# Performance work log

Hardware: AMD Instinct MI355X
Metric: run time of the kernel (lower is better)

Reference implementation:

```python
import jax, jax.numpy as jnp
import numpy as np

K = 3          # kernel_size
STRIDE = 1
ITERS = 3      # num_iterations


def squash(t, axis=-1):
    sn = jnp.sum(t * t, axis=axis, keepdims=True)
    return (sn / (1.0 + sn)) * t / jnp.sqrt(sn)


def setup_inputs() -> dict:
    key = jax.random.key(0)
    k1, k2 = jax.random.split(key)
    B, Nin, H, Cin = 8, 32, 14, 8
    C, Cout = 32, 16
    R = Nin * K * K  # 288 route nodes
    x = jax.random.normal(k1, (B, Nin, H, H, Cin), dtype=jnp.float32)
    route_weights = jax.random.normal(k2, (C, R, Cin, Cout), dtype=jnp.float32)
    return {"x": x, "route_weights": route_weights}


def reference(x, route_weights):
    B, Nin, H, _, Cin = x.shape
    C, R, _, Cout = route_weights.shape
    w = (H - K) // STRIDE + 1

    # Extract all w*w spatial windows at once (instead of the python loop).
    rows = STRIDE * jnp.arange(w)[:, None] + jnp.arange(K)  # [w, K]
    win = x[:, :, rows]            # [B, Nin, w, K, W, Cin]
    win = win[:, :, :, :, rows]    # [B, Nin, w, K, w, K, Cin]
    # route-node order matches .view: (Nin, k, k) flattened
    win = win.transpose(0, 2, 4, 1, 3, 5, 6).reshape(B, w, w, R, Cin)

    priors = jnp.einsum('bpqri,crio->cbpqro', win, route_weights)

    # Dynamic routing (fixed small iteration count -> python loop is fine).
    logits = jnp.zeros_like(priors)
    out = None
    for i in range(ITERS):
        probs = jax.nn.softmax(logits, axis=4)  # softmax over route nodes (dim=2 in torch 5D layout)
        out = squash(jnp.sum(probs * priors, axis=4, keepdims=True))  # [C,B,w,w,1,Cout]
        if i != ITERS - 1:
            logits = logits + jnp.sum(priors * out, axis=-1, keepdims=True)

    out = out[:, :, :, :, 0, :]          # [C, B, w, w, Cout]
    return out.transpose(1, 0, 2, 3, 4)  # [B, C, w, w, Cout]
```

## Files before the change

kernel.cpp:

```cpp
#include <hip/hip_runtime.h>
#include <math.h>

namespace {
constexpr int NIN   = 32;
constexpr int H_    = 14;
constexpr int CIN   = 8;
constexpr int C_    = 32;
constexpr int COUT  = 16;
constexpr int R_    = 288;
constexpr int W_    = 12;
constexpr int NITER = 3;
constexpr int CH    = 32;
constexpr int NCH   = 9;
constexpr size_t XSUB = (size_t)NIN * H_ * H_ * CIN;
}

typedef unsigned int u32;
typedef const __attribute__((address_space(1))) u32* as1_u32p;
typedef __attribute__((address_space(3))) u32* as3_u32p;

__device__ __forceinline__ void async_copy16(const void* g, void* l) {
    __builtin_amdgcn_global_load_lds((as1_u32p)g, (as3_u32p)l, 16, 0, 0);
}
__device__ __forceinline__ float dot4(const float4 a, const float4 b) {
    return fmaf(a.x, b.x, fmaf(a.y, b.y, fmaf(a.z, b.z, a.w * b.w)));
}
__device__ __forceinline__ float dpp_add_xor1(float v) {
    int t = __builtin_amdgcn_update_dpp(0, __float_as_int(v), 0xB1, 0xF, 0xF, true);
    return v + __int_as_float(t);
}
__device__ __forceinline__ float dpp_add_xor2(float v) {
    int t = __builtin_amdgcn_update_dpp(0, __float_as_int(v), 0x4E, 0xF, 0xF, true);
    return v + __int_as_float(t);
}
__device__ __forceinline__ float dpp_add_shr4(float v) {
    int t = __builtin_amdgcn_update_dpp(0, __float_as_int(v), 0x114, 0xF, 0xF, true);
    return v + __int_as_float(t);
}
__device__ __forceinline__ float dpp_add_shr8(float v) {
    int t = __builtin_amdgcn_update_dpp(0, __float_as_int(v), 0x118, 0xF, 0xF, true);
    return v + __int_as_float(t);
}
template <int CTRL>
__device__ __forceinline__ float dpp_bc(float v) {
    return __int_as_float(
        __builtin_amdgcn_update_dpp(0, __float_as_int(v), CTRL, 0xF, 0xF, true));
}

__global__ __launch_bounds__(256)
void caps_routeC(const float* __restrict__ x,
                 const float* __restrict__ rw,
                 float* __restrict__ out)
{
    const int tid = threadIdx.x;
    const int p  = blockIdx.x / W_;
    const int q  = blockIdx.x % W_;
    const int b0 = blockIdx.y * 4;
    const int c  = blockIdx.z;

    __shared__ float4 wbuf[2][1024];
    __shared__ float  sRed[2][4][2][16];
    __shared__ float  redE[2][4][2];

    const int og   = tid & 3;
    const int rl   = tid >> 2;
    const int cr   = rl & 31;
    const int sh   = rl >> 5;
    const int lane = tid & 63;
    const int wv   = tid >> 6;
    const int sA   = sh * 2;

    const float* xq = x + (size_t)(b0 + sA + (og >> 1)) * XSUB + (og & 1) * 4;
    const float4* rwcF4 = (const float4*)(rw + (size_t)c * R_ * CIN * COUT);

    float4 xvb[2];
    auto xld = [&](int k, int slot) {
        const int r  = k * CH + cr;
        const int n  = r / 9, rem = r - n * 9;
        const int kh = rem / 3, kw = rem - kh * 3;
        xvb[slot] = *(const float4*)(xq + ((n * H_ + (p + kh)) * H_ + (q + kw)) * CIN);
    };

    auto stage = [&](int k, int buf) {
        const float4* gchunk = rwcF4 + (size_t)k * (CH * 32);
        #pragma unroll
        for (int t = 0; t < 4; ++t) {
            const int s   = t * 256 + tid;
            const int ii  = s >> 7;
            const int wcr = (s >> 2) & 31;
            async_copy16(gchunk + (wcr * 32 + ii * 4 + (s & 3)),
                         (char*)&wbuf[buf][0] + (t * 256 + (tid & 192)) * 16);
        }
    };

    float4 acc[NCH][2];

    xld(0, 0);
    xld(1, 1);
    stage(0, 0);
    #pragma unroll
    for (int k = 0; k < NCH; ++k) {
        __syncthreads();
        if (k + 1 < NCH) stage(k + 1, (k + 1) & 1);
        const float4 cur = xvb[k & 1];
        float fA[8], fB[8];
        fA[0] = dpp_bc<0x00>(cur.x); fA[1] = dpp_bc<0x00>(cur.y);
        fA[2] = dpp_bc<0x00>(cur.z); fA[3] = dpp_bc<0x00>(cur.w);
        fA[4] = dpp_bc<0x55>(cur.x); fA[5] = dpp_bc<0x55>(cur.y);
        fA[6] = dpp_bc<0x55>(cur.z); fA[7] = dpp_bc<0x55>(cur.w);
        fB[0] = dpp_bc<0xAA>(cur.x); fB[1] = dpp_bc<0xAA>(cur.y);
        fB[2] = dpp_bc<0xAA>(cur.z); fB[3] = dpp_bc<0xAA>(cur.w);
        fB[4] = dpp_bc<0xFF>(cur.x); fB[5] = dpp_bc<0xFF>(cur.y);
        fB[6] = dpp_bc<0xFF>(cur.z); fB[7] = dpp_bc<0xFF>(cur.w);
        if (k + 2 < NCH) xld(k + 2, k & 1);
        const float4* wb = &wbuf[k & 1][0];
        float4 a0 = make_float4(0.f, 0.f, 0.f, 0.f);
        float4 a1 = make_float4(0.f, 0.f, 0.f, 0.f);
        #pragma unroll
        for (int i = 0; i < 8; ++i) {
            const float4 wv4 = wb[i * 128 + cr * 4 + og];
            a0.x = fmaf(fA[i], wv4.x, a0.x);  a1.x = fmaf(fB[i], wv4.x, a1.x);
            a0.y = fmaf(fA[i], wv4.y, a0.y);  a1.y = fmaf(fB[i], wv4.y, a1.y);
            a0.z = fmaf(fA[i], wv4.z, a0.z);  a1.z = fmaf(fB[i], wv4.z, a1.z);
            a0.w = fmaf(fA[i], wv4.w, a0.w);  a1.w = fmaf(fB[i], wv4.w, a1.w);
        }
        acc[k][0] = a0;  acc[k][1] = a1;
    }

    float lgA[NCH], lgB[NCH];
    #pragma unroll
    for (int j = 0; j < NCH; ++j) { lgA[j] = 0.f; lgB[j] = 0.f; }

    float4 v0, v1;

    for (int it = 0; it < NITER; ++it) {
        const int par = it & 1;
        float4 s0 = make_float4(0.f, 0.f, 0.f, 0.f);
        float4 s1 = make_float4(0.f, 0.f, 0.f, 0.f);
        float se0 = 0.f, se1 = 0.f;

        if (it == 0) {
            #pragma unroll
            for (int j = 0; j < NCH; ++j) {
                s0.x += acc[j][0].x;  s1.x += acc[j][1].x;
                s0.y += acc[j][0].y;  s1.y += acc[j][1].y;
                s0.z += acc[j][0].z;  s1.z += acc[j][1].z;
                s0.w += acc[j][0].w;  s1.w += acc[j][1].w;
            }
        } else {
            #pragma unroll
            for (int j = 0; j < NCH; ++j) {
                float d0 = dot4(acc[j][0], v0);
                float d1 = dot4(acc[j][1], v1);
                d0 = dpp_add_xor1(d0);  d1 = dpp_add_xor1(d1);
                d0 = dpp_add_xor2(d0);  d1 = dpp_add_xor2(d1);
                lgA[j] += d0;                 lgB[j] += d1;
                const float e0 = __expf(lgA[j]);
                const float e1 = __expf(lgB[j]);
                se0 += e0;                    se1 += e1;
                s0.x = fmaf(e0, acc[j][0].x, s0.x);  s1.x = fmaf(e1, acc[j][1].x, s1.x);
                s0.y = fmaf(e0, acc[j][0].y, s0.y);  s1.y = fmaf(e1, acc[j][1].y, s1.y);
                s0.z = fmaf(e0, acc[j][0].z, s0.z);  s1.z = fmaf(e1, acc[j][1].z, s1.z);
                s0.w = fmaf(e0, acc[j][0].w, s0.w);  s1.w = fmaf(e1, acc[j][1].w, s1.w);
            }
            se0 = dpp_add_shr4(se0);  se1 = dpp_add_shr4(se1);
            se0 = dpp_add_shr8(se0);  se1 = dpp_add_shr8(se1);
            se0 += __shfl_xor(se0, 16, 64);  se1 += __shfl_xor(se1, 16, 64);
            se0 += __shfl_xor(se0, 32, 64);  se1 += __shfl_xor(se1, 32, 64);
            if (lane == 15) { redE[par][wv][0] = se0; redE[par][wv][1] = se1; }
        }

        s0.x = dpp_add_shr4(s0.x);  s1.x = dpp_add_shr4(s1.x);
        s0.y = dpp_add_shr4(s0.y);  s1.y = dpp_add_shr4(s1.y);
        s0.z = dpp_add_shr4(s0.z);  s1.z = dpp_add_shr4(s1.z);
        s0.w = dpp_add_shr4(s0.w);  s1.w = dpp_add_shr4(s1.w);
        s0.x = dpp_add_shr8(s0.x);  s1.x = dpp_add_shr8(s1.x);
        s0.y = dpp_add_shr8(s0.y);  s1.y = dpp_add_shr8(s1.y);
        s0.z = dpp_add_shr8(s0.z);  s1.z = dpp_add_shr8(s1.z);
        s0.w = dpp_add_shr8(s0.w);  s1.w = dpp_add_shr8(s1.w);
        #pragma unroll
        for (int off = 16; off <= 32; off <<= 1) {
            s0.x += __shfl_xor(s0.x, off, 64);  s1.x += __shfl_xor(s1.x, off, 64);
            s0.y += __shfl_xor(s0.y, off, 64);  s1.y += __shfl_xor(s1.y, off, 64);
            s0.z += __shfl_xor(s0.z, off, 64);  s1.z += __shfl_xor(s1.z, off, 64);
            s0.w += __shfl_xor(s0.w, off, 64);  s1.w += __shfl_xor(s1.w, off, 64);
        }
        if (lane >= 12 && lane < 16) {
            *(float4*)&sRed[par][wv][0][(lane & 3) * 4] = s0;
            *(float4*)&sRed[par][wv][1][(lane & 3) * 4] = s1;
        }
        __syncthreads();

        const float4 pa0 = *(const float4*)&sRed[par][sh * 2    ][0][og * 4];
        const float4 pb0 = *(const float4*)&sRed[par][sh * 2 + 1][0][og * 4];
        const float4 pa1 = *(const float4*)&sRed[par][sh * 2    ][1][og * 4];
        const float4 pb1 = *(const float4*)&sRed[par][sh * 2 + 1][1][og * 4];
        float inv0, inv1;
        if (it == 0) {
            inv0 = inv1 = 1.0f / (float)R_;
        } else {
            inv0 = 1.0f / (redE[par][sh * 2][0] + redE[par][sh * 2 + 1][0]);
            inv1 = 1.0f / (redE[par][sh * 2][1] + redE[par][sh * 2 + 1][1]);
        }
        float4 sc0, sc1;
        sc0.x = (pa0.x + pb0.x) * inv0;  sc1.x = (pa1.x + pb1.x) * inv1;
        sc0.y = (pa0.y + pb0.y) * inv0;  sc1.y = (pa1.y + pb1.y) * inv1;
        sc0.z = (pa0.z + pb0.z) * inv0;  sc1.z = (pa1.z + pb1.z) * inv1;
        sc0.w = (pa0.w + pb0.w) * inv0;  sc1.w = (pa1.w + pb1.w) * inv1;
        float sn0 = dot4(sc0, sc0);
        float sn1 = dot4(sc1, sc1);
        sn0 = dpp_add_xor1(sn0);  sn1 = dpp_add_xor1(sn1);
        sn0 = dpp_add_xor2(sn0);  sn1 = dpp_add_xor2(sn1);
        const float f0 = sqrtf(sn0) / (1.0f + sn0);
        const float f1 = sqrtf(sn1) / (1.0f + sn1);
        v0.x = sc0.x * f0;  v1.x = sc1.x * f1;
        v0.y = sc0.y * f0;  v1.y = sc1.y * f1;
        v0.z = sc0.z * f0;  v1.z = sc1.z * f1;
        v0.w = sc0.w * f0;  v1.w = sc1.w * f1;
    }

    if (cr == 0) {
        *(float4*)&out[((((size_t)(b0 + sA)     * C_ + c) * W_ + p) * W_ + q) * COUT + og * 4] = v0;
        *(float4*)&out[((((size_t)(b0 + sA + 1) * C_ + c) * W_ + p) * W_ + q) * COUT + og * 4] = v1;
    }
}

extern "C" void kernel_launch(void* const* d_in, const int* in_sizes, int n_in,
                              void* d_out, int out_size, void* d_ws, size_t ws_size,
                              hipStream_t stream) {
    const float* x  = (const float*)d_in[0];
    const float* rw = (const float*)d_in[1];
    float* out = (float*)d_out;
    dim3 grid(W_ * W_, 2, C_);
    caps_routeC<<<grid, 256, 0, stream>>>(x, rw, out);
}
```

Before: 197.9 us.

## Deepen weight staging to a five-buffer half-chunk pipeline with explicit vmcnt waits

The weight staging loop is split into 18 half-chunks held in a 5-slot shared-memory ring with four stages in flight. Hand-tuned s_waitcnt vmcnt values and raw s_barrier calls replace __syncthreads, and sched_barrier fences pin the instruction order. The aim is to hide global-to-LDS load latency behind the FMA work with less stalling per barrier. The reduction scratch now aliases the ring buffer, and the hard-coded wait counts depend on the exact order the compiler emits memory instructions, so a codegen change could break correctness.

```diff
diff --git a/kernel.cpp b/kernel.cpp
--- a/kernel.cpp
+++ b/kernel.cpp
@@ -12,6 +12,7 @@
 constexpr int NITER = 3;
 constexpr int CH    = 32;
 constexpr int NCH   = 9;
+constexpr int NPH   = 18;
 constexpr size_t XSUB = (size_t)NIN * H_ * H_ * CIN;
 }
 
@@ -58,9 +59,9 @@
     const int b0 = blockIdx.y * 4;
     const int c  = blockIdx.z;
 
-    __shared__ float4 wbuf[2][1024];
-    __shared__ float  sRed[2][4][2][16];
-    __shared__ float  redE[2][4][2];
+    __shared__ __align__(16) char smem[40960];
+    float (*sRedP)[4][2][16] = reinterpret_cast<float (*)[4][2][16]>(smem);
+    float (*redEP)[4][2]     = reinterpret_cast<float (*)[4][2]>(smem + 1024);
 
     const int og   = tid & 3;
     const int rl   = tid >> 2;
@@ -81,50 +82,73 @@
         xvb[slot] = *(const float4*)(xq + ((n * H_ + (p + kh)) * H_ + (q + kw)) * CIN);
     };
 
-    auto stage = [&](int k, int buf) {
+    auto stage = [&](int h) {
+        const int k = h >> 1, half = h & 1, buf = h % 5;
         const float4* gchunk = rwcF4 + (size_t)k * (CH * 32);
         #pragma unroll
-        for (int t = 0; t < 4; ++t) {
+        for (int t = 0; t < 2; ++t) {
             const int s   = t * 256 + tid;
             const int ii  = s >> 7;
             const int wcr = (s >> 2) & 31;
-            async_copy16(gchunk + (wcr * 32 + ii * 4 + (s & 3)),
-                         (char*)&wbuf[buf][0] + (t * 256 + (tid & 192)) * 16);
+            async_copy16(gchunk + (wcr * 32 + (half * 4 + ii) * 4 + (s & 3)),
+                         smem + buf * 8192 + (t * 256 + (tid & 192)) * 16);
         }
     };
 
+    constexpr int NWAIT[NPH] = {6,7,7,8, 7,8,7,8, 7,8,7,8, 7,9,8,6, 2,0};
+    auto vwait = [](int n) {
+        switch (n) {
+          case 2: asm volatile("s_waitcnt vmcnt(2) lgkmcnt(0)" ::: "memory"); break;
+          case 6: asm volatile("s_waitcnt vmcnt(6) lgkmcnt(0)" ::: "memory"); break;
+          case 7: asm volatile("s_waitcnt vmcnt(7) lgkmcnt(0)" ::: "memory"); break;
+          case 8: asm volatile("s_waitcnt vmcnt(8) lgkmcnt(0)" ::: "memory"); break;
+          case 9: asm volatile("s_waitcnt vmcnt(9) lgkmcnt(0)" ::: "memory"); break;
+          default: asm volatile("s_waitcnt vmcnt(0) lgkmcnt(0)" ::: "memory"); break;
+        }
+    };
+
     float4 acc[NCH][2];
+    float  fA[8], fB[8];
+    float4 a0, a1;
 
     xld(0, 0);
-    xld(1, 1);
-    stage(0, 0);
+    stage(0); stage(1); stage(2); stage(3);
     #pragma unroll
-    for (int k = 0; k < NCH; ++k) {
-        __syncthreads();
-        if (k + 1 < NCH) stage(k + 1, (k + 1) & 1);
-        const float4 cur = xvb[k & 1];
-        float fA[8], fB[8];
-        fA[0] = dpp_bc<0x00>(cur.x); fA[1] = dpp_bc<0x00>(cur.y);
-        fA[2] = dpp_bc<0x00>(cur.z); fA[3] = dpp_bc<0x00>(cur.w);
-        fA[4] = dpp_bc<0x55>(cur.x); fA[5] = dpp_bc<0x55>(cur.y);
-        fA[6] = dpp_bc<0x55>(cur.z); fA[7] = dpp_bc<0x55>(cur.w);
-        fB[0] = dpp_bc<0xAA>(cur.x); fB[1] = dpp_bc<0xAA>(cur.y);
-        fB[2] = dpp_bc<0xAA>(cur.z); fB[3] = dpp_bc<0xAA>(cur.w);
-        fB[4] = dpp_bc<0xFF>(cur.x); fB[5] = dpp_bc<0xFF>(cur.y);
-        fB[6] = dpp_bc<0xFF>(cur.z); fB[7] = dpp_bc<0xFF>(cur.w);
-        if (k + 2 < NCH) xld(k + 2, k & 1);
-        const float4* wb = &wbuf[k & 1][0];
-        float4 a0 = make_float4(0.f, 0.f, 0.f, 0.f);
-        float4 a1 = make_float4(0.f, 0.f, 0.f, 0.f);
+    for (int h = 0; h < NPH; ++h) {
+        const int k = h >> 1, half = h & 1;
+        vwait(NWAIT[h]);
+        __builtin_amdgcn_s_barrier();
+        __builtin_amdgcn_sched_barrier(0);
+        if (half == 0) {
+            const float4 cur = xvb[k & 1];
+            fA[0] = dpp_bc<0x00>(cur.x); fA[1] = dpp_bc<0x00>(cur.y);
+            fA[2] = dpp_bc<0x00>(cur.z); fA[3] = dpp_bc<0x00>(cur.w);
+            fA[4] = dpp_bc<0x55>(cur.x); fA[5] = dpp_bc<0x55>(cur.y);
+            fA[6] = dpp_bc<0x55>(cur.z); fA[7] = dpp_bc<0x55>(cur.w);
+            fB[0] = dpp_bc<0xAA>(cur.x); fB[1] = dpp_bc<0xAA>(cur.y);
+            fB[2] = dpp_bc<0xAA>(cur.z); fB[3] = dpp_bc<0xAA>(cur.w);
+            fB[4] = dpp_bc<0xFF>(cur.x); fB[5] = dpp_bc<0xFF>(cur.y);
+            fB[6] = dpp_bc<0xFF>(cur.z); fB[7] = dpp_bc<0xFF>(cur.w);
+            if (k + 1 < 8) xld(k + 1, (k + 1) & 1);
+            if (k == 6)    xld(8, 0);
+            a0 = make_float4(0.f, 0.f, 0.f, 0.f);
+            a1 = make_float4(0.f, 0.f, 0.f, 0.f);
+        }
+        __builtin_amdgcn_sched_barrier(0);
+        if (h + 4 < NPH) stage(h + 4);
+        __builtin_amdgcn_sched_barrier(0);
+        const float4* wb = (const float4*)(smem + (h % 5) * 8192);
         #pragma unroll
-        for (int i = 0; i < 8; ++i) {
-            const float4 wv4 = wb[i * 128 + cr * 4 + og];
-            a0.x = fmaf(fA[i], wv4.x, a0.x);  a1.x = fmaf(fB[i], wv4.x, a1.x);
-            a0.y = fmaf(fA[i], wv4.y, a0.y);  a1.y = fmaf(fB[i], wv4.y, a1.y);
-            a0.z = fmaf(fA[i], wv4.z, a0.z);  a1.z = fmaf(fB[i], wv4.z, a1.z);
-            a0.w = fmaf(fA[i], wv4.w, a0.w);  a1.w = fmaf(fB[i], wv4.w, a1.w);
-        }
-        acc[k][0] = a0;  acc[k][1] = a1;
+        for (int ii = 0; ii < 4; ++ii) {
+            const float fa = fA[half * 4 + ii];
+            const float fb = fB[half * 4 + ii];
+            const float4 wv4 = wb[ii * 128 + cr * 4 + og];
+            a0.x = fmaf(fa, wv4.x, a0.x);  a1.x = fmaf(fb, wv4.x, a1.x);
+            a0.y = fmaf(fa, wv4.y, a0.y);  a1.y = fmaf(fb, wv4.y, a1.y);
+            a0.z = fmaf(fa, wv4.z, a0.z);  a1.z = fmaf(fb, wv4.z, a1.z);
+            a0.w = fmaf(fa, wv4.w, a0.w);  a1.w = fmaf(fb, wv4.w, a1.w);
+        }
+        if (half == 1) { acc[k][0] = a0;  acc[k][1] = a1; }
     }
 
     float lgA[NCH], lgB[NCH];
@@ -167,7 +191,7 @@
             se0 = dpp_add_shr8(se0);  se1 = dpp_add_shr8(se1);
             se0 += __shfl_xor(se0, 16, 64);  se1 += __shfl_xor(se1, 16, 64);
             se0 += __shfl_xor(se0, 32, 64);  se1 += __shfl_xor(se1, 32, 64);
-            if (lane == 15) { redE[par][wv][0] = se0; redE[par][wv][1] = se1; }
+            if (lane == 15) { redEP[par][wv][0] = se0; redEP[par][wv][1] = se1; }
         }
 
         s0.x = dpp_add_shr4(s0.x);  s1.x = dpp_add_shr4(s1.x);
@@ -186,21 +210,21 @@
             s0.w += __shfl_xor(s0.w, off, 64);  s1.w += __shfl_xor(s1.w, off, 64);
         }
         if (lane >= 12 && lane < 16) {
-            *(float4*)&sRed[par][wv][0][(lane & 3) * 4] = s0;
-            *(float4*)&sRed[par][wv][1][(lane & 3) * 4] = s1;
+            *(float4*)&sRedP[par][wv][0][(lane & 3) * 4] = s0;
+            *(float4*)&sRedP[par][wv][1][(lane & 3) * 4] = s1;
         }
         __syncthreads();
 
-        const float4 pa0 = *(const float4*)&sRed[par][sh * 2    ][0][og * 4];
-        const float4 pb0 = *(const float4*)&sRed[par][sh * 2 + 1][0][og * 4];
-        const float4 pa1 = *(const float4*)&sRed[par][sh * 2    ][1][og * 4];
-        const float4 pb1 = *(const float4*)&sRed[par][sh * 2 + 1][1][og * 4];
+        const float4 pa0 = *(const float4*)&sRedP[par][sh * 2    ][0][og * 4];
+        const float4 pb0 = *(const float4*)&sRedP[par][sh * 2 + 1][0][og * 4];
+        const float4 pa1 = *(const float4*)&sRedP[par][sh * 2    ][1][og * 4];
+        const float4 pb1 = *(const float4*)&sRedP[par][sh * 2 + 1][1][og * 4];
         float inv0, inv1;
         if (it == 0) {
             inv0 = inv1 = 1.0f / (float)R_;
         } else {
-            inv0 = 1.0f / (redE[par][sh * 2][0] + redE[par][sh * 2 + 1][0]);
-            inv1 = 1.0f / (redE[par][sh * 2][1] + redE[par][sh * 2 + 1][1]);
+            inv0 = 1.0f / (redEP[par][sh * 2][0] + redEP[par][sh * 2 + 1][0]);
+            inv1 = 1.0f / (redEP[par][sh * 2][1] + redEP[par][sh * 2 + 1][1]);
         }
         float4 sc0, sc1;
         sc0.x = (pa0.x + pb0.x) * inv0;  sc1.x = (pa1.x + pb1.x) * inv1;
```

Result: slower. 255.7 us (+29.2%).
